# Optimization experiments

Measured on AMD Instinct MI355X. Metric: run time of the kernel, lower is better.

## Reference

```python
import jax, jax.numpy as jnp
import numpy as np

B, H0, W0, C, NH, WS, SHIFT = 32, 48, 48, 384, 12, 12, 6
N = WS * WS
TAB = 2 * WS - 1  # 23


def _window_partition(x, ws):
    b, h, w, c = x.shape
    x = x.reshape(b, h // ws, ws, w // ws, ws, c)
    return x.transpose(0, 1, 3, 2, 4, 5).reshape(-1, ws, ws, c)


def _window_reverse(win, ws, h, w):
    b = win.shape[0] // (h * w // ws // ws)
    x = win.reshape(b, h // ws, w // ws, ws, ws, -1)
    return x.transpose(0, 1, 3, 2, 4, 5).reshape(b, h, w, -1)


def _ln(y, g, b):
    m = y.mean(-1, keepdims=True)
    v = y.var(-1, keepdims=True)
    return (y - m) * jax.lax.rsqrt(v + 1e-5) * g + b


def setup_inputs() -> dict:
    key = jax.random.key(0)
    ks = jax.random.split(key, 12)
    s = 0.02
    # relative coords table, normalized to [-1, 1]
    rng = np.arange(-(WS - 1), WS, dtype=np.float32) / (WS - 1)
    table = np.stack(np.meshgrid(rng, rng, indexing='ij'), axis=-1)[None]  # (1,23,23,2)
    # relative position index
    ch, cw = np.meshgrid(np.arange(WS), np.arange(WS), indexing='ij')
    coords = np.stack([ch, cw]).reshape(2, -1)
    rel = coords[:, :, None] - coords[:, None, :] + (WS - 1)
    rpi = (rel[0] * TAB + rel[1]).astype(np.int32)  # (N,N)
    # shifted-window attention mask
    img = np.zeros((1, H0, W0, 1), dtype=np.float32)
    cnt = 0
    sl = (slice(0, -WS), slice(-WS, -SHIFT), slice(-SHIFT, None))
    for hs in sl:
        for ws_ in sl:
            img[:, hs, ws_, :] = cnt
            cnt += 1
    mw = img.reshape(1, H0 // WS, WS, W0 // WS, WS, 1).transpose(0, 1, 3, 2, 4, 5).reshape(-1, N)
    diff = mw[:, None, :] - mw[:, :, None]
    attn_mask = np.where(diff != 0, -100.0, 0.0).astype(np.float32)  # (nW,N,N)
    Ch = C * 4
    return {
        'x': jax.random.normal(ks[0], (B, H0 * W0, C), jnp.float32),
        'relative_coords_table': jnp.asarray(table),
        'relative_position_index': jnp.asarray(rpi),
        'attn_mask': jnp.asarray(attn_mask),
        'qkv_w': jax.random.normal(ks[1], (C, 3 * C), jnp.float32) * s,
        'q_bias': jnp.zeros((C,), jnp.float32),
        'v_bias': jnp.zeros((C,), jnp.float32),
        'logit_scale': jnp.log(10.0 * jnp.ones((NH, 1, 1), jnp.float32)),
        'cpb_w1': jax.random.normal(ks[2], (2, 512), jnp.float32) * s,
        'cpb_b1': jnp.zeros((512,), jnp.float32),
        'cpb_w2': jax.random.normal(ks[3], (512, NH), jnp.float32) * s,
        'proj_w': jax.random.normal(ks[4], (C, C), jnp.float32) * s,
        'proj_b': jnp.zeros((C,), jnp.float32),
        'norm1_g': jnp.ones((C,), jnp.float32),
        'norm1_b': jnp.zeros((C,), jnp.float32),
        'norm2_g': jnp.ones((C,), jnp.float32),
        'norm2_b': jnp.zeros((C,), jnp.float32),
        'fc1_w': jax.random.normal(ks[5], (C, Ch), jnp.float32) * s,
        'fc1_b': jnp.zeros((Ch,), jnp.float32),
        'fc2_w': jax.random.normal(ks[6], (Ch, C), jnp.float32) * s,
        'fc2_b': jnp.zeros((C,), jnp.float32),
        'H': H0,
        'W': W0,
    }


def reference(x, relative_coords_table, relative_position_index, attn_mask,
              qkv_w, q_bias, v_bias, logit_scale, cpb_w1, cpb_b1, cpb_w2,
              proj_w, proj_b, norm1_g, norm1_b, norm2_g, norm2_b,
              fc1_w, fc1_b, fc2_w, fc2_b, H, W):
    b, L, c = x.shape
    hd = c // NH
    shortcut = x
    x4 = x.reshape(b, H, W, c)
    shifted = jnp.roll(x4, (-SHIFT, -SHIFT), axis=(1, 2))
    xw = _window_partition(shifted, WS).reshape(-1, N, c)  # (B_, N, C)
    qkv_bias = jnp.concatenate([q_bias, jnp.zeros_like(q_bias), v_bias])
    qkv = xw @ qkv_w + qkv_bias
    qkv = qkv.reshape(-1, N, 3, NH, hd).transpose(2, 0, 3, 1, 4)  # (3,B_,h,N,d)
    q, k, v = qkv[0], qkv[1], qkv[2]
    qn = q / jnp.maximum(jnp.linalg.norm(q, axis=-1, keepdims=True), 1e-12)
    kn = k / jnp.maximum(jnp.linalg.norm(k, axis=-1, keepdims=True), 1e-12)
    attn = jnp.einsum('bhnd,bhmd->bhnm', qn, kn)
    scale = jnp.exp(jnp.minimum(logit_scale, jnp.log(100.0)))  # clamp max=log(1/0.01)
    attn = attn * scale
    tab = jax.nn.relu(relative_coords_table @ cpb_w1 + cpb_b1) @ cpb_w2  # (1,23,23,h)
    tab = tab.reshape(-1, NH)
    bias = tab[relative_position_index.reshape(-1)].reshape(N, N, NH).transpose(2, 0, 1)
    bias = 16.0 * jax.nn.sigmoid(bias)
    attn = attn + bias[None]
    nW = attn_mask.shape[0]
    attn = attn.reshape(b, nW, NH, N, N) + attn_mask[None, :, None]
    attn = jax.nn.softmax(attn.reshape(-1, NH, N, N), axis=-1)
    out = jnp.einsum('bhnm,bhmd->bhnd', attn, v).transpose(0, 2, 1, 3).reshape(-1, N, c)
    out = out @ proj_w + proj_b
    out = _window_reverse(out.reshape(-1, WS, WS, c), WS, H, W)
    x4 = jnp.roll(out, (SHIFT, SHIFT), axis=(1, 2)).reshape(b, H * W, c)
    x = shortcut + _ln(x4, norm1_g, norm1_b)
    h = jax.nn.gelu(x @ fc1_w + fc1_b, approximate=False) @ fc2_w + fc2_b
    x = x + _ln(h, norm2_g, norm2_b)
    return x
```

## Files before the change

### kernel.cpp

```cpp
#include <hip/hip_runtime.h>


typedef unsigned int uint32;
typedef unsigned short u16;
typedef __attribute__((ext_vector_type(4))) float f32x4;
typedef __attribute__((ext_vector_type(8))) __bf16 bf16x8;

static __device__ __forceinline__ u16 f2bf(float f) {
    union { float f; uint32 u; } v; v.f = f;
    uint32 r = v.u + 0x7fffu + ((v.u >> 16) & 1u);
    return (u16)(r >> 16);
}
static __device__ __forceinline__ float bf2f(u16 h) {
    union { uint32 u; float f; } v; v.u = ((uint32)h) << 16; return v.f;
}
static __device__ __forceinline__ uint32 pack2(float a, float b) {
    return (uint32)f2bf(a) | ((uint32)f2bf(b) << 16);
}
static __device__ __forceinline__ float blo(uint32 u){ union{uint32 u;float f;}v; v.u=u<<16; return v.f; }
static __device__ __forceinline__ float bhi(uint32 u){ union{uint32 u;float f;}v; v.u=u&0xffff0000u; return v.f; }

typedef __attribute__((address_space(1))) const void gas_void;
typedef __attribute__((address_space(3))) void las_void;
static __device__ __forceinline__ void glds16(const void* g, void* l) {
    __builtin_amdgcn_global_load_lds((gas_void*)g, (las_void*)l, 16, 0, 0);
}

#define SWZ(c, row) ((c) ^ ((((row) >> 1) & 3) << 3))

static __device__ __forceinline__ float fast_gelu(float x) {
    float z = x * 0.70710678118654752f;
    float az = fabsf(z);
    float t = __builtin_amdgcn_rcpf(fmaf(0.3275911f, az, 1.0f));
    float p = t * (0.254829592f + t * (-0.284496736f + t * (1.421413741f
              + t * (-1.453152027f + t * 1.061405429f))));
    float e = __expf(-z * z);
    float er = copysignf(fmaf(-p, e, 1.0f), z);
    return 0.5f * x * (1.0f + er);
}


__global__ void wt_convert(const float* __restrict__ W, u16* __restrict__ WT, int K, int N) {
    long idx = (long)blockIdx.x * 256 + threadIdx.x;
    long tot = (long)K * N;
    if (idx >= tot) return;
    int n = (int)(idx / K), k = (int)(idx - (long)n * K);
    WT[(long)n * K + SWZ(k, n)] = f2bf(W[(long)k * N + n]);
}

__global__ void build_qkv_bias(const float* __restrict__ qb, const float* __restrict__ vb,
                               float* __restrict__ outb) {
    int c = blockIdx.x * 256 + threadIdx.x;
    if (c >= 1152) return;
    outb[c] = (c < 384) ? qb[c] : ((c < 768) ? 0.f : vb[c - 768]);
}

__global__ void cpb_tab(const float* __restrict__ table, const float* __restrict__ w1,
                        const float* __restrict__ b1, const float* __restrict__ w2,
                        float* __restrict__ tab) {
    __shared__ float hid[512];
    int e = blockIdx.x;
    float tx = table[e * 2 + 0], ty = table[e * 2 + 1];
    for (int u = threadIdx.x; u < 512; u += 256)
        hid[u] = fmaxf(tx * w1[u] + ty * w1[512 + u] + b1[u], 0.f);
    __syncthreads();
    if (threadIdx.x < 12) {
        float s = 0.f;
        for (int u = 0; u < 512; ++u) s += hid[u] * w2[u * 12 + threadIdx.x];
        tab[e * 12 + threadIdx.x] = s;
    }
}

__global__ void cpb_bias(const float* __restrict__ tab, const int* __restrict__ rpi,
                         float* __restrict__ bias16) {
    int idx = blockIdx.x * 256 + threadIdx.x;
    if (idx >= 12 * 144 * 144) return;
    int h = idx / 20736, ij = idx - h * 20736;
    float t = tab[rpi[ij] * 12 + h];
    bias16[idx] = 16.f / (1.f + __expf(-t));
}

__global__ void gather_xbf(const float* __restrict__ x, u16* __restrict__ xw) {
    int idx = blockIdx.x * 256 + threadIdx.x;
    if (idx >= 73728 * 48) return;
    int row = idx / 48, c = (idx - row * 48) * 8;
    int win = row / 144, n = row - win * 144;
    int b = win >> 4, wi = win & 15;
    int r = n / 12, cc = n - r * 12;
    int sh = ((wi >> 2) * 12 + r + 6) % 48;
    int sw = ((wi & 3) * 12 + cc + 6) % 48;
    long src = ((long)(b * 2304 + sh * 48 + sw)) * 384 + c;
    float4 f0 = *(const float4*)(x + src);
    float4 f1 = *(const float4*)(x + src + 4);
    uint4 o;
    o.x = pack2(f0.x, f0.y); o.y = pack2(f0.z, f0.w);
    o.z = pack2(f1.x, f1.y); o.w = pack2(f1.z, f1.w);
    *(uint4*)(xw + (long)row * 384 + SWZ(c, row)) = o;
}


enum { EPI_QKV = 0, EPI_PLAIN = 1, EPI_GELU = 2 };

template<int EPI, bool OSWZ>
__global__ __launch_bounds__(256) void gemm_k(
    const u16* __restrict__ Ag, const u16* __restrict__ Bg,
    const float* __restrict__ bias, u16* __restrict__ outp,
    int N, int K, int ntn)
{
    __shared__ __align__(16) u16 As[2][128 * 32];
    __shared__ __align__(16) u16 Bs[2][128 * 32];
    const int tid = threadIdx.x, lane = tid & 63, wid = tid >> 6;
    const int qq = gridDim.x >> 3;
    const int wg = (blockIdx.x & 7) * qq + (blockIdx.x >> 3);
    const int mIdx = wg / ntn, nIdx = wg - mIdx * ntn;
    const int m0 = mIdx << 7, n0 = nIdx << 7;

    const int wrow = (wid >> 1) << 6, wcol = (wid & 1) << 6;
    const int fr = lane & 15, gsel = lane >> 4;

    const int s_r = (wid << 5) + (lane >> 2);
    const int s_g = (lane & 3) << 3;
    const long a_base = (long)(m0 + s_r) * K + s_g;
    const long b_base = (long)(n0 + s_r) * K + s_g;
    const long qstep = (long)16 * K;

    auto stage = [&](int buf, int kt) {
        const int k0 = kt << 5;
#pragma unroll
        for (int q = 0; q < 2; ++q) {
            glds16(Ag + a_base + qstep * q + k0, &As[buf][(wid * 32 + q * 16) * 32]);
            glds16(Bg + b_base + qstep * q + k0, &Bs[buf][(wid * 32 + q * 16) * 32]);
        }
    };

    int arow[4], acol[4], brow[4], bcol[4];
#pragma unroll
    for (int i = 0; i < 4; ++i) {
        arow[i] = wrow + i * 16 + fr; acol[i] = SWZ(gsel * 8, arow[i]);
        brow[i] = wcol + i * 16 + fr; bcol[i] = SWZ(gsel * 8, brow[i]);
    }

    f32x4 acc[4][4];
    const f32x4 zero4 = {0.f, 0.f, 0.f, 0.f};
#pragma unroll
    for (int i = 0; i < 4; ++i)
#pragma unroll
        for (int j = 0; j < 4; ++j) acc[i][j] = zero4;

    const int nk = K >> 5;
    stage(0, 0);
    int cur = 0;
    for (int kt = 0; kt < nk; ++kt) {
        __syncthreads();
        if (kt + 1 < nk) stage(cur ^ 1, kt + 1);
        bf16x8 af[4], bg[4];
#pragma unroll
        for (int i = 0; i < 4; ++i) af[i] = *(const bf16x8*)&As[cur][arow[i] * 32 + acol[i]];
#pragma unroll
        for (int j = 0; j < 4; ++j) bg[j] = *(const bf16x8*)&Bs[cur][brow[j] * 32 + bcol[j]];
#pragma unroll
        for (int i = 0; i < 4; ++i)
#pragma unroll
            for (int j = 0; j < 4; ++j)
                acc[i][j] = __builtin_amdgcn_mfma_f32_16x16x32_bf16(af[i], bg[j], acc[i][j], 0, 0, 0);
        cur ^= 1;
    }

    const int rbase = (lane >> 4) << 2;
    if constexpr (EPI == EPI_QKV) {
        long coloff[4];
        float bv[4];
#pragma unroll
        for (int j = 0; j < 4; ++j) {
            int gn0 = n0 + wcol + j * 16;
            int which = gn0 / 384;
            int c = gn0 - which * 384;
            coloff[j] = (long)(which * 12 + (c >> 5)) * 4608 + (c & 31);
            bv[j] = bias[gn0 + fr];
        }
#pragma unroll
        for (int i = 0; i < 4; ++i) {
            long rowoff[4];
#pragma unroll
            for (int r = 0; r < 4; ++r) {
                int gm = m0 + wrow + i * 16 + rbase + r;
                int win = gm / 144, n = gm - win * 144;
                rowoff[r] = (long)win * 165888 + n * 32;
            }
#pragma unroll
            for (int j = 0; j < 4; ++j)
#pragma unroll
                for (int r = 0; r < 4; ++r)
                    outp[rowoff[r] + coloff[j] + fr] = f2bf(acc[i][j][r] + bv[j]);
        }
    } else {
        float bv[4];
#pragma unroll
        for (int j = 0; j < 4; ++j) bv[j] = bias[n0 + wcol + j * 16 + fr];
#pragma unroll
        for (int i = 0; i < 4; ++i) {
#pragma unroll
            for (int r = 0; r < 4; ++r) {
                const int gm = m0 + wrow + i * 16 + rbase + r;
                u16* orow = outp + (long)gm * N;
                const int sx = OSWZ ? (((gm >> 1) & 3) << 3) : 0;
#pragma unroll
                for (int j = 0; j < 4; ++j) {
                    const int gn = n0 + wcol + j * 16 + fr;
                    float v = acc[i][j][r] + bv[j];
                    if constexpr (EPI == EPI_GELU) v = fast_gelu(v);
                    orow[gn ^ sx] = f2bf(v);
                }
            }
        }
    }
}


__global__ __launch_bounds__(192) void attn_k(
    const u16* __restrict__ qkv,
    const float* __restrict__ bias16,
    const float* __restrict__ mask,
    const float* __restrict__ lsc,
    u16* __restrict__ attn_o)
{
    __shared__ __align__(16) u16 KL[144][40];
    __shared__ __align__(16) u16 VT[32][168];
    __shared__ __align__(16) u16 PL[3][16][168];
    const int blk = blockIdx.x;
    const int win = blk / 12, head = blk - win * 12;
    const int tid = threadIdx.x, lane = tid & 63, wid = tid >> 6;
    const long base = ((long)win * 36 + head) * 4608;
    const u16* Qp = qkv + base;
    const u16* Kp = qkv + base + 12 * 4608;
    const u16* Vp = qkv + base + 24 * 4608;
    const float scale = __expf(fminf(lsc[head], 4.6051701859880914f));

    if (tid < 144) {
        const uint4* s = (const uint4*)(Kp + tid * 32);
        uint4 uu[4] = { s[0], s[1], s[2], s[3] };
        float f[32];
#pragma unroll
        for (int q = 0; q < 4; ++q) {
            f[q*8+0]=blo(uu[q].x); f[q*8+1]=bhi(uu[q].x);
            f[q*8+2]=blo(uu[q].y); f[q*8+3]=bhi(uu[q].y);
            f[q*8+4]=blo(uu[q].z); f[q*8+5]=bhi(uu[q].z);
            f[q*8+6]=blo(uu[q].w); f[q*8+7]=bhi(uu[q].w);
        }
        float ss = 0.f;
#pragma unroll
        for (int i = 0; i < 32; ++i) ss += f[i] * f[i];
        float inv = 1.f / fmaxf(sqrtf(ss), 1e-12f);
        uint32 pk[16];
#pragma unroll
        for (int i = 0; i < 16; ++i) pk[i] = pack2(f[2*i] * inv, f[2*i+1] * inv);
        uint4* d = (uint4*)&KL[tid][0];
        d[0] = make_uint4(pk[0], pk[1], pk[2], pk[3]);
        d[1] = make_uint4(pk[4], pk[5], pk[6], pk[7]);
        d[2] = make_uint4(pk[8], pk[9], pk[10], pk[11]);
        d[3] = make_uint4(pk[12], pk[13], pk[14], pk[15]);
        const uint4* sv = (const uint4*)(Vp + tid * 32);
        uint4 vv[4] = { sv[0], sv[1], sv[2], sv[3] };
        u16 vs[32];
#pragma unroll
        for (int q = 0; q < 4; ++q) {
            vs[q*8+0] = (u16)(vv[q].x & 0xffffu); vs[q*8+1] = (u16)(vv[q].x >> 16);
            vs[q*8+2] = (u16)(vv[q].y & 0xffffu); vs[q*8+3] = (u16)(vv[q].y >> 16);
            vs[q*8+4] = (u16)(vv[q].z & 0xffffu); vs[q*8+5] = (u16)(vv[q].z >> 16);
            vs[q*8+6] = (u16)(vv[q].w & 0xffffu); vs[q*8+7] = (u16)(vv[q].w >> 16);
        }
#pragma unroll
        for (int d2 = 0; d2 < 32; ++d2) VT[d2][tid] = vs[d2];
    }
    for (int idx = tid; idx < 512; idx += 192) VT[idx >> 4][144 + (idx & 15)] = 0;
    __syncthreads();

    const int fr = lane & 15, fk = (lane >> 4) << 3, rb = (lane >> 4) << 2;
    const int wim = win & 15;
    const f32x4 zero4 = {0.f, 0.f, 0.f, 0.f};

    for (int s = wid; s < 9; s += 3) {
        const uint4 qu = *(const uint4*)(Qp + (s * 16 + fr) * 32 + fk);
        float qf[8];
        qf[0]=blo(qu.x); qf[1]=bhi(qu.x); qf[2]=blo(qu.y); qf[3]=bhi(qu.y);
        qf[4]=blo(qu.z); qf[5]=bhi(qu.z); qf[6]=blo(qu.w); qf[7]=bhi(qu.w);
        float ss = 0.f;
#pragma unroll
        for (int i = 0; i < 8; ++i) ss += qf[i] * qf[i];
        ss += __shfl_xor(ss, 16);
        ss += __shfl_xor(ss, 32);
        float qinv = scale / fmaxf(sqrtf(ss), 1e-12f);
        union { uint32 u[4]; bf16x8 v; } cv;
#pragma unroll
        for (int i = 0; i < 4; ++i) cv.u[i] = pack2(qf[2*i] * qinv, qf[2*i+1] * qinv);
        bf16x8 aq = cv.v;

        f32x4 sacc[9];
#pragma unroll
        for (int jt = 0; jt < 9; ++jt) sacc[jt] = zero4;
#pragma unroll
        for (int jt = 0; jt < 9; ++jt) {
            bf16x8 bk = *(const bf16x8*)&KL[jt * 16 + fr][fk];
            sacc[jt] = __builtin_amdgcn_mfma_f32_16x16x32_bf16(aq, bk, sacc[jt], 0, 0, 0);
        }
        float mx[4] = {-1e30f, -1e30f, -1e30f, -1e30f};
#pragma unroll
        for (int jt = 0; jt < 9; ++jt) {
            int gj = jt * 16 + fr;
#pragma unroll
            for (int r = 0; r < 4; ++r) {
                int gi = s * 16 + rb + r;
                float v = sacc[jt][r] + bias16[(head * 144 + gi) * 144 + gj]
                                      + mask[(wim * 144 + gi) * 144 + gj];
                sacc[jt][r] = v;
                mx[r] = fmaxf(mx[r], v);
            }
        }
#pragma unroll
        for (int r = 0; r < 4; ++r) {
#pragma unroll
            for (int o = 1; o < 16; o <<= 1) mx[r] = fmaxf(mx[r], __shfl_xor(mx[r], o));
        }
        float sm[4] = {0.f, 0.f, 0.f, 0.f};
#pragma unroll
        for (int jt = 0; jt < 9; ++jt)
#pragma unroll
            for (int r = 0; r < 4; ++r) {
                float e = __expf(sacc[jt][r] - mx[r]);
                sacc[jt][r] = e;
                sm[r] += e;
            }
#pragma unroll
        for (int r = 0; r < 4; ++r) {
#pragma unroll
            for (int o = 1; o < 16; o <<= 1) sm[r] += __shfl_xor(sm[r], o);
            sm[r] = 1.f / sm[r];
        }
#pragma unroll
        for (int jt = 0; jt < 9; ++jt)
#pragma unroll
            for (int r = 0; r < 4; ++r)
                PL[wid][rb + r][jt * 16 + fr] = f2bf(sacc[jt][r]);
#pragma unroll
        for (int r = 0; r < 4; ++r) PL[wid][rb + r][144 + fr] = 0;

        f32x4 oa0 = zero4, oa1 = zero4;
#pragma unroll
        for (int kt = 0; kt < 5; ++kt) {
            bf16x8 ap  = *(const bf16x8*)&PL[wid][fr][kt * 32 + fk];
            bf16x8 bv0 = *(const bf16x8*)&VT[fr][kt * 32 + fk];
            bf16x8 bv1 = *(const bf16x8*)&VT[16 + fr][kt * 32 + fk];
            oa0 = __builtin_amdgcn_mfma_f32_16x16x32_bf16(ap, bv0, oa0, 0, 0, 0);
            oa1 = __builtin_amdgcn_mfma_f32_16x16x32_bf16(ap, bv1, oa1, 0, 0, 0);
        }
#pragma unroll
        for (int r = 0; r < 4; ++r) {
            long row = (long)win * 144 + s * 16 + rb + r;
            int c0 = head * 32 + fr, c1 = head * 32 + 16 + fr;
            attn_o[row * 384 + SWZ(c0, row)] = f2bf(oa0[r] * sm[r]);
            attn_o[row * 384 + SWZ(c1, row)] = f2bf(oa1[r] * sm[r]);
        }
    }
}


__global__ __launch_bounds__(256) void ln1_k(
    const u16* __restrict__ pin, const float* __restrict__ x,
    const float* __restrict__ g, const float* __restrict__ bb,
    u16* __restrict__ y1b)
{
    const int token = blockIdx.x * 4 + (threadIdx.x >> 6);
    const int lane = threadIdx.x & 63;
    int b = token / 2304, hw = token - b * 2304;
    int h = hw / 48, w = hw - h * 48;
    int sh = h + 42; if (sh >= 48) sh -= 48;
    int sw = w + 42; if (sw >= 48) sw -= 48;
    int wh = sh / 12, r = sh - wh * 12;
    int ww = sw / 12, cc = sw - ww * 12;
    long srow = (long)(b * 16 + wh * 4 + ww) * 144 + r * 12 + cc;
    const u16* src = pin + srow * 384;
    float v[6];
    {
        const ushort2* s2 = (const ushort2*)src;
#pragma unroll
        for (int i = 0; i < 3; ++i) {
            ushort2 p = s2[lane * 3 + i];
            v[i * 2] = bf2f(p.x); v[i * 2 + 1] = bf2f(p.y);
        }
    }
    float s1 = 0.f, s2 = 0.f;
#pragma unroll
    for (int i = 0; i < 6; ++i) { s1 += v[i]; s2 += v[i] * v[i]; }
#pragma unroll
    for (int o = 1; o < 64; o <<= 1) { s1 += __shfl_xor(s1, o); s2 += __shfl_xor(s2, o); }
    float mean = s1 * (1.f / 384.f);
    float var = s2 * (1.f / 384.f) - mean * mean;
    float rs = rsqrtf(var + 1e-5f);
    const float* rr = x + (long)token * 384;
    u16* oo = y1b + (long)token * 384;
#pragma unroll
    for (int i = 0; i < 6; ++i) {
        int c = lane * 6 + i;
        oo[SWZ(c, token)] = f2bf(rr[c] + (v[i] - mean) * rs * g[c] + bb[c]);
    }
}

__global__ __launch_bounds__(256) void ln2_k(
    const u16* __restrict__ t2, const u16* __restrict__ y1b,
    const float* __restrict__ g, const float* __restrict__ bb,
    float* __restrict__ outp)
{
    const int token = blockIdx.x * 4 + (threadIdx.x >> 6);
    const int lane = threadIdx.x & 63;
    const u16* src = t2 + (long)token * 384;
    float v[6];
    {
        const ushort2* s2 = (const ushort2*)src;
#pragma unroll
        for (int i = 0; i < 3; ++i) {
            ushort2 p = s2[lane * 3 + i];
            v[i * 2] = bf2f(p.x); v[i * 2 + 1] = bf2f(p.y);
        }
    }
    float s1 = 0.f, s2 = 0.f;
#pragma unroll
    for (int i = 0; i < 6; ++i) { s1 += v[i]; s2 += v[i] * v[i]; }
#pragma unroll
    for (int o = 1; o < 64; o <<= 1) { s1 += __shfl_xor(s1, o); s2 += __shfl_xor(s2, o); }
    float mean = s1 * (1.f / 384.f);
    float var = s2 * (1.f / 384.f) - mean * mean;
    float rs = rsqrtf(var + 1e-5f);
    const u16* rr = y1b + (long)token * 384;
    float* oo = outp + (long)token * 384;
#pragma unroll
    for (int i = 0; i < 6; ++i) {
        int c = lane * 6 + i;
        oo[c] = bf2f(rr[SWZ(c, token)]) + (v[i] - mean) * rs * g[c] + bb[c];
    }
}


extern "C" void kernel_launch(void* const* d_in, const int* in_sizes, int n_in,
                              void* d_out, int out_size, void* d_ws, size_t ws_size,
                              hipStream_t stream) {
    (void)in_sizes; (void)n_in; (void)out_size; (void)ws_size;
    const float* x      = (const float*)d_in[0];
    const float* table  = (const float*)d_in[1];
    const int*   rpi    = (const int*)d_in[2];
    const float* mask   = (const float*)d_in[3];
    const float* qkv_w  = (const float*)d_in[4];
    const float* q_bias = (const float*)d_in[5];
    const float* v_bias = (const float*)d_in[6];
    const float* lsc    = (const float*)d_in[7];
    const float* cpb_w1 = (const float*)d_in[8];
    const float* cpb_b1 = (const float*)d_in[9];
    const float* cpb_w2 = (const float*)d_in[10];
    const float* proj_w = (const float*)d_in[11];
    const float* proj_b = (const float*)d_in[12];
    const float* n1g    = (const float*)d_in[13];
    const float* n1b    = (const float*)d_in[14];
    const float* n2g    = (const float*)d_in[15];
    const float* n2b    = (const float*)d_in[16];
    const float* fc1_w  = (const float*)d_in[17];
    const float* fc1_b  = (const float*)d_in[18];
    const float* fc2_w  = (const float*)d_in[19];
    const float* fc2_b  = (const float*)d_in[20];
    float* outp = (float*)d_out;

    char* ws = (char*)d_ws;
    const size_t offA    = 0;
    const size_t offB    = 226492416;
    const size_t offC    = offB + 56623104;
    const size_t offBias = offC + 56623104;
    const size_t offTab  = offBias + 995328;
    const size_t offQW   = offTab + 25600;
    const size_t offPW   = offQW + 884736;
    const size_t offF1   = offPW + 294912;
    const size_t offF2   = offF1 + 1179648;
    const size_t offQB   = offF2 + 1179648;

    u16*   qkvb    = (u16*)(ws + offA);
    u16*   proj_o  = (u16*)(ws + offA);
    u16*   hbuf    = (u16*)(ws + offA);
    u16*   attn_o  = (u16*)(ws + offB);
    u16*   t2      = (u16*)(ws + offB);
    u16*   xw      = (u16*)(ws + offC);
    u16*   y1b     = (u16*)(ws + offC);
    float* bias16  = (float*)(ws + offBias);
    float* tab     = (float*)(ws + offTab);
    u16*   qkv_wT  = (u16*)(ws + offQW);
    u16*   proj_wT = (u16*)(ws + offPW);
    u16*   fc1_wT  = (u16*)(ws + offF1);
    u16*   fc2_wT  = (u16*)(ws + offF2);
    float* qkvbias = (float*)(ws + offQB);

    wt_convert<<<(384 * 1152 + 255) / 256, 256, 0, stream>>>(qkv_w, qkv_wT, 384, 1152);
    wt_convert<<<(384 * 384 + 255) / 256, 256, 0, stream>>>(proj_w, proj_wT, 384, 384);
    wt_convert<<<(384 * 1536 + 255) / 256, 256, 0, stream>>>(fc1_w, fc1_wT, 384, 1536);
    wt_convert<<<(1536 * 384 + 255) / 256, 256, 0, stream>>>(fc2_w, fc2_wT, 1536, 384);
    build_qkv_bias<<<5, 256, 0, stream>>>(q_bias, v_bias, qkvbias);
    cpb_tab<<<529, 256, 0, stream>>>(table, cpb_w1, cpb_b1, cpb_w2, tab);
    cpb_bias<<<(12 * 144 * 144 + 255) / 256, 256, 0, stream>>>(tab, rpi, bias16);
    gather_xbf<<<(73728 * 48 + 255) / 256, 256, 0, stream>>>(x, xw);

    gemm_k<EPI_QKV, false><<<576 * 9, 256, 0, stream>>>(xw, qkv_wT, qkvbias, qkvb, 1152, 384, 9);

    attn_k<<<6144, 192, 0, stream>>>(qkvb, bias16, mask, lsc, attn_o);

    gemm_k<EPI_PLAIN, false><<<576 * 3, 256, 0, stream>>>(attn_o, proj_wT, proj_b, proj_o, 384, 384, 3);

    ln1_k<<<18432, 256, 0, stream>>>(proj_o, x, n1g, n1b, y1b);

    gemm_k<EPI_GELU, true><<<576 * 12, 256, 0, stream>>>(y1b, fc1_wT, fc1_b, hbuf, 1536, 384, 12);

    gemm_k<EPI_PLAIN, false><<<576 * 3, 256, 0, stream>>>(hbuf, fc2_wT, fc2_b, t2, 384, 1536, 3);

    ln2_k<<<18432, 256, 0, stream>>>(t2, y1b, n2g, n2b, outp);
}
```

Before: 816.8 us.

## Replace GEMM with 256x256-tile 8-wave pipelined kernel and padded weights

```diff
diff --git a/kernel.cpp b/kernel.cpp
--- a/kernel.cpp
+++ b/kernel.cpp
@@ -26,7 +26,10 @@
     __builtin_amdgcn_global_load_lds((gas_void*)g, (las_void*)l, 16, 0, 0);
 }
 
-#define SWZ(c, row) ((c) ^ ((((row) >> 1) & 3) << 3))
+#define SWZ(c, row) ((c) ^ (((row) & 7) << 3))
+
+#define VMCNT(N) asm volatile("s_waitcnt vmcnt(" #N ")" ::: "memory")
+#define BARM() do { asm volatile("" ::: "memory"); __builtin_amdgcn_s_barrier(); asm volatile("" ::: "memory"); } while (0)
 
 static __device__ __forceinline__ float fast_gelu(float x) {
     float z = x * 0.70710678118654752f;
@@ -40,19 +43,21 @@
 }
 
 
-__global__ void wt_convert(const float* __restrict__ W, u16* __restrict__ WT, int K, int N) {
+__global__ void wt_convert(const float* __restrict__ W, u16* __restrict__ WT,
+                           int K, int Nreal, int Npad) {
     long idx = (long)blockIdx.x * 256 + threadIdx.x;
-    long tot = (long)K * N;
+    long tot = (long)K * Npad;
     if (idx >= tot) return;
     int n = (int)(idx / K), k = (int)(idx - (long)n * K);
-    WT[(long)n * K + SWZ(k, n)] = f2bf(W[(long)k * N + n]);
+    float v = (n < Nreal) ? W[(long)k * Nreal + n] : 0.f;
+    WT[(long)n * K + SWZ(k, n)] = f2bf(v);
 }
 
 __global__ void build_qkv_bias(const float* __restrict__ qb, const float* __restrict__ vb,
                                float* __restrict__ outb) {
     int c = blockIdx.x * 256 + threadIdx.x;
-    if (c >= 1152) return;
-    outb[c] = (c < 384) ? qb[c] : ((c < 768) ? 0.f : vb[c - 768]);
+    if (c >= 1280) return;
+    outb[c] = (c < 384) ? qb[c] : ((c < 768) ? 0.f : (c < 1152 ? vb[c - 768] : 0.f));
 }
 
 __global__ void cpb_tab(const float* __restrict__ table, const float* __restrict__ w1,
@@ -102,118 +107,156 @@
 enum { EPI_QKV = 0, EPI_PLAIN = 1, EPI_GELU = 2 };
 
 template<int EPI, bool OSWZ>
-__global__ __launch_bounds__(256) void gemm_k(
+__global__ __launch_bounds__(512, 2) void gemm8(
     const u16* __restrict__ Ag, const u16* __restrict__ Bg,
     const float* __restrict__ bias, u16* __restrict__ outp,
-    int N, int K, int ntn)
+    int Nout, int K, int ntn)
 {
-    __shared__ __align__(16) u16 As[2][128 * 32];
-    __shared__ __align__(16) u16 Bs[2][128 * 32];
+    extern __shared__ u16 lds[];
     const int tid = threadIdx.x, lane = tid & 63, wid = tid >> 6;
     const int qq = gridDim.x >> 3;
     const int wg = (blockIdx.x & 7) * qq + (blockIdx.x >> 3);
     const int mIdx = wg / ntn, nIdx = wg - mIdx * ntn;
-    const int m0 = mIdx << 7, n0 = nIdx << 7;
-
-    const int wrow = (wid >> 1) << 6, wcol = (wid & 1) << 6;
+    const int m0 = mIdx << 8, n0 = nIdx << 8;
+    const int wr = wid >> 2, wc = wid & 3;
     const int fr = lane & 15, gsel = lane >> 4;
-
-    const int s_r = (wid << 5) + (lane >> 2);
-    const int s_g = (lane & 3) << 3;
-    const long a_base = (long)(m0 + s_r) * K + s_g;
-    const long b_base = (long)(n0 + s_r) * K + s_g;
-    const long qstep = (long)16 * K;
-
-    auto stage = [&](int buf, int kt) {
-        const int k0 = kt << 5;
-#pragma unroll
-        for (int q = 0; q < 2; ++q) {
-            glds16(Ag + a_base + qstep * q + k0, &As[buf][(wid * 32 + q * 16) * 32]);
-            glds16(Bg + b_base + qstep * q + k0, &Bs[buf][(wid * 32 + q * 16) * 32]);
+    const int sx = (fr & 7) << 3;
+
+    bf16x8 a[4][2], b[2][2];
+    f32x4 acc00[4][2], acc01[4][2], acc10[4][2], acc11[4][2];
+    const f32x4 z4 = {0.f, 0.f, 0.f, 0.f};
+#pragma unroll
+    for (int i = 0; i < 4; ++i)
+#pragma unroll
+        for (int j = 0; j < 2; ++j) { acc00[i][j] = z4; acc01[i][j] = z4; acc10[i][j] = z4; acc11[i][j] = z4; }
+
+    auto STA = [&](int buf, int t, int half) {
+#pragma unroll
+        for (int u = 0; u < 2; ++u) {
+            const int g = (wid << 1) + u;
+            const int rin = half * 128 + (g << 3) + (lane >> 3);
+            glds16(Ag + (long)(m0 + rin) * K + (t << 6) + ((lane & 7) << 3),
+                   &lds[buf * 16384 + (half * 128 + (g << 3)) * 64]);
         }
     };
-
-    int arow[4], acol[4], brow[4], bcol[4];
-#pragma unroll
-    for (int i = 0; i < 4; ++i) {
-        arow[i] = wrow + i * 16 + fr; acol[i] = SWZ(gsel * 8, arow[i]);
-        brow[i] = wcol + i * 16 + fr; bcol[i] = SWZ(gsel * 8, brow[i]);
-    }
-
-    f32x4 acc[4][4];
-    const f32x4 zero4 = {0.f, 0.f, 0.f, 0.f};
-#pragma unroll
-    for (int i = 0; i < 4; ++i)
-#pragma unroll
-        for (int j = 0; j < 4; ++j) acc[i][j] = zero4;
-
-    const int nk = K >> 5;
-    stage(0, 0);
-    int cur = 0;
-    for (int kt = 0; kt < nk; ++kt) {
-        __syncthreads();
-        if (kt + 1 < nk) stage(cur ^ 1, kt + 1);
-        bf16x8 af[4], bg[4];
-#pragma unroll
-        for (int i = 0; i < 4; ++i) af[i] = *(const bf16x8*)&As[cur][arow[i] * 32 + acol[i]];
-#pragma unroll
-        for (int j = 0; j < 4; ++j) bg[j] = *(const bf16x8*)&Bs[cur][brow[j] * 32 + bcol[j]];
+    auto STB = [&](int buf, int t, int half) {
+#pragma unroll
+        for (int u = 0; u < 2; ++u) {
+            const int g = (wid << 1) + u;
+            const int rin = half * 128 + (g << 3) + (lane >> 3);
+            glds16(Bg + (long)(n0 + rin) * K + (t << 6) + ((lane & 7) << 3),
+                   &lds[32768 + buf * 16384 + (half * 128 + (g << 3)) * 64]);
+        }
+    };
+    auto RDA = [&](int buf, int mh) {
+        const int rb = mh * 128 + wr * 64 + fr;
+#pragma unroll
+        for (int i = 0; i < 4; ++i) {
+            const int r = rb + i * 16;
+#pragma unroll
+            for (int kk = 0; kk < 2; ++kk)
+                a[i][kk] = *(const bf16x8*)&lds[buf * 16384 + r * 64 + (((kk << 5) | (gsel << 3)) ^ sx)];
+        }
+    };
+    auto RDB = [&](int buf, int nh) {
+        const int rb = nh * 128 + wc * 32 + fr;
+#pragma unroll
+        for (int j = 0; j < 2; ++j) {
+            const int r = rb + j * 16;
+#pragma unroll
+            for (int kk = 0; kk < 2; ++kk)
+                b[j][kk] = *(const bf16x8*)&lds[32768 + buf * 16384 + r * 64 + (((kk << 5) | (gsel << 3)) ^ sx)];
+        }
+    };
+    auto MM = [&](f32x4 (&cc)[4][2]) {
+        __builtin_amdgcn_s_setprio(1);
 #pragma unroll
         for (int i = 0; i < 4; ++i)
 #pragma unroll
-            for (int j = 0; j < 4; ++j)
-                acc[i][j] = __builtin_amdgcn_mfma_f32_16x16x32_bf16(af[i], bg[j], acc[i][j], 0, 0, 0);
-        cur ^= 1;
-    }
-
-    const int rbase = (lane >> 4) << 2;
-    if constexpr (EPI == EPI_QKV) {
-        long coloff[4];
-        float bv[4];
-#pragma unroll
-        for (int j = 0; j < 4; ++j) {
-            int gn0 = n0 + wcol + j * 16;
-            int which = gn0 / 384;
-            int c = gn0 - which * 384;
-            coloff[j] = (long)(which * 12 + (c >> 5)) * 4608 + (c & 31);
-            bv[j] = bias[gn0 + fr];
+            for (int j = 0; j < 2; ++j)
+#pragma unroll
+                for (int kk = 0; kk < 2; ++kk)
+                    cc[i][j] = __builtin_amdgcn_mfma_f32_16x16x32_bf16(a[i][kk], b[j][kk], cc[i][j], 0, 0, 0);
+        __builtin_amdgcn_s_setprio(0);
+    };
+
+#define GITER(T, S5, W5, W6, W7)                                   \
+    STA(1, (T) + 1, 0); VMCNT(6); BARM();                          \
+    RDA(0, 0); RDB(0, 0); MM(acc00);                               \
+    STB(1, (T) + 1, 0); VMCNT(6); BARM();                          \
+    RDB(0, 1); MM(acc01);                                          \
+    STB(1, (T) + 1, 1); VMCNT(6); BARM();                          \
+    RDA(0, 1); MM(acc11);                                          \
+    STA(1, (T) + 1, 1); VMCNT(6); BARM();                          \
+    RDB(0, 0); MM(acc10);                                          \
+    if (S5) STA(0, (T) + 2, 0);                                    \
+    W5; BARM();                                                    \
+    RDA(1, 0); RDB(1, 0); MM(acc00);                               \
+    if (S5) STB(0, (T) + 2, 0);                                    \
+    W6; BARM();                                                    \
+    RDB(1, 1); MM(acc01);                                          \
+    if (S5) STB(0, (T) + 2, 1);                                    \
+    W7; BARM();                                                    \
+    RDA(1, 1); MM(acc11);                                          \
+    if (S5) STA(0, (T) + 2, 1);                                    \
+    BARM();                                                        \
+    RDB(1, 0); MM(acc10);
+
+    STA(0, 0, 0); STB(0, 0, 0); STB(0, 0, 1); STA(0, 0, 1);
+    const int niter = K >> 7;
+    for (int it = 0; it < niter - 1; ++it) {
+        const int t = it << 1;
+        GITER(t, true, VMCNT(6), VMCNT(6), VMCNT(6));
+    }
+    {
+        const int t = (niter - 1) << 1;
+        GITER(t, false, VMCNT(4), VMCNT(2), VMCNT(0));
+    }
+#undef GITER
+
+    const int rb4 = gsel << 2;
+    auto EPIL = [&](f32x4 (&cc)[4][2], int mh, int nh) {
+        int gn0[2]; bool inb[2]; float bv[2]; long coloff[2];
+#pragma unroll
+        for (int j = 0; j < 2; ++j) {
+            gn0[j] = n0 + nh * 128 + wc * 32 + j * 16;
+            inb[j] = gn0[j] < Nout;
+            bv[j] = inb[j] ? bias[gn0[j] + fr] : 0.f;
+            if (EPI == EPI_QKV && inb[j]) {
+                int which = gn0[j] / 384;
+                int c0 = gn0[j] - which * 384;
+                coloff[j] = (long)(which * 12 + (c0 >> 5)) * 4608 + (c0 & 31) + fr;
+            }
         }
 #pragma unroll
         for (int i = 0; i < 4; ++i) {
-            long rowoff[4];
 #pragma unroll
             for (int r = 0; r < 4; ++r) {
-                int gm = m0 + wrow + i * 16 + rbase + r;
-                int win = gm / 144, n = gm - win * 144;
-                rowoff[r] = (long)win * 165888 + n * 32;
-            }
-#pragma unroll
-            for (int j = 0; j < 4; ++j)
-#pragma unroll
-                for (int r = 0; r < 4; ++r)
-                    outp[rowoff[r] + coloff[j] + fr] = f2bf(acc[i][j][r] + bv[j]);
-        }
-    } else {
-        float bv[4];
-#pragma unroll
-        for (int j = 0; j < 4; ++j) bv[j] = bias[n0 + wcol + j * 16 + fr];
-#pragma unroll
-        for (int i = 0; i < 4; ++i) {
-#pragma unroll
-            for (int r = 0; r < 4; ++r) {
-                const int gm = m0 + wrow + i * 16 + rbase + r;
-                u16* orow = outp + (long)gm * N;
-                const int sx = OSWZ ? (((gm >> 1) & 3) << 3) : 0;
-#pragma unroll
-                for (int j = 0; j < 4; ++j) {
-                    const int gn = n0 + wcol + j * 16 + fr;
-                    float v = acc[i][j][r] + bv[j];
-                    if constexpr (EPI == EPI_GELU) v = fast_gelu(v);
-                    orow[gn ^ sx] = f2bf(v);
+                const int gm = m0 + mh * 128 + wr * 64 + i * 16 + rb4 + r;
+                if constexpr (EPI == EPI_QKV) {
+                    const int win = gm / 144, n = gm - win * 144;
+                    const long rowbase = (long)win * 165888 + n * 32;
+#pragma unroll
+                    for (int j = 0; j < 2; ++j)
+                        if (inb[j]) outp[rowbase + coloff[j]] = f2bf(cc[i][j][r] + bv[j]);
+                } else {
+                    u16* orow = outp + (long)gm * Nout;
+                    const int sxo = OSWZ ? ((gm & 7) << 3) : 0;
+#pragma unroll
+                    for (int j = 0; j < 2; ++j) {
+                        if (!inb[j]) continue;
+                        float v = cc[i][j][r] + bv[j];
+                        if constexpr (EPI == EPI_GELU) v = fast_gelu(v);
+                        orow[(gn0[j] + fr) ^ sxo] = f2bf(v);
+                    }
                 }
             }
         }
-    }
+    };
+    EPIL(acc00, 0, 0);
+    EPIL(acc01, 0, 1);
+    EPIL(acc10, 1, 0);
+    EPIL(acc11, 1, 1);
 }
 
 
@@ -474,10 +517,10 @@
     const size_t offBias = offC + 56623104;
     const size_t offTab  = offBias + 995328;
     const size_t offQW   = offTab + 25600;
-    const size_t offPW   = offQW + 884736;
-    const size_t offF1   = offPW + 294912;
+    const size_t offPW   = offQW + 983040;
+    const size_t offF1   = offPW + 393216;
     const size_t offF2   = offF1 + 1179648;
-    const size_t offQB   = offF2 + 1179648;
+    const size_t offQB   = offF2 + 1572864;
 
     u16*   qkvb    = (u16*)(ws + offA);
     u16*   proj_o  = (u16*)(ws + offA);
@@ -494,26 +537,33 @@
     u16*   fc2_wT  = (u16*)(ws + offF2);
     float* qkvbias = (float*)(ws + offQB);
 
-    wt_convert<<<(384 * 1152 + 255) / 256, 256, 0, stream>>>(qkv_w, qkv_wT, 384, 1152);
-    wt_convert<<<(384 * 384 + 255) / 256, 256, 0, stream>>>(proj_w, proj_wT, 384, 384);
-    wt_convert<<<(384 * 1536 + 255) / 256, 256, 0, stream>>>(fc1_w, fc1_wT, 384, 1536);
-    wt_convert<<<(1536 * 384 + 255) / 256, 256, 0, stream>>>(fc2_w, fc2_wT, 1536, 384);
+    hipFuncSetAttribute((const void*)&gemm8<EPI_QKV, false>,
+                        hipFuncAttributeMaxDynamicSharedMemorySize, 131072);
+    hipFuncSetAttribute((const void*)&gemm8<EPI_PLAIN, false>,
+                        hipFuncAttributeMaxDynamicSharedMemorySize, 131072);
+    hipFuncSetAttribute((const void*)&gemm8<EPI_GELU, true>,
+                        hipFuncAttributeMaxDynamicSharedMemorySize, 131072);
+
+    wt_convert<<<(384 * 1280 + 255) / 256, 256, 0, stream>>>(qkv_w, qkv_wT, 384, 1152, 1280);
+    wt_convert<<<(384 * 512 + 255) / 256, 256, 0, stream>>>(proj_w, proj_wT, 384, 384, 512);
+    wt_convert<<<(384 * 1536 + 255) / 256, 256, 0, stream>>>(fc1_w, fc1_wT, 384, 1536, 1536);
+    wt_convert<<<(1536 * 512 + 255) / 256, 256, 0, stream>>>(fc2_w, fc2_wT, 1536, 384, 512);
     build_qkv_bias<<<5, 256, 0, stream>>>(q_bias, v_bias, qkvbias);
     cpb_tab<<<529, 256, 0, stream>>>(table, cpb_w1, cpb_b1, cpb_w2, tab);
     cpb_bias<<<(12 * 144 * 144 + 255) / 256, 256, 0, stream>>>(tab, rpi, bias16);
     gather_xbf<<<(73728 * 48 + 255) / 256, 256, 0, stream>>>(x, xw);
 
-    gemm_k<EPI_QKV, false><<<576 * 9, 256, 0, stream>>>(xw, qkv_wT, qkvbias, qkvb, 1152, 384, 9);
+    gemm8<EPI_QKV, false><<<288 * 5, 512, 131072, stream>>>(xw, qkv_wT, qkvbias, qkvb, 1152, 384, 5);
 
     attn_k<<<6144, 192, 0, stream>>>(qkvb, bias16, mask, lsc, attn_o);
 
-    gemm_k<EPI_PLAIN, false><<<576 * 3, 256, 0, stream>>>(attn_o, proj_wT, proj_b, proj_o, 384, 384, 3);
+    gemm8<EPI_PLAIN, false><<<288 * 2, 512, 131072, stream>>>(attn_o, proj_wT, proj_b, proj_o, 384, 384, 2);
 
     ln1_k<<<18432, 256, 0, stream>>>(proj_o, x, n1g, n1b, y1b);
 
-    gemm_k<EPI_GELU, true><<<576 * 12, 256, 0, stream>>>(y1b, fc1_wT, fc1_b, hbuf, 1536, 384, 12);
-
-    gemm_k<EPI_PLAIN, false><<<576 * 3, 256, 0, stream>>>(hbuf, fc2_wT, fc2_b, t2, 384, 1536, 3);
+    gemm8<EPI_GELU, true><<<288 * 6, 512, 131072, stream>>>(y1b, fc1_wT, fc1_b, hbuf, 1536, 384, 6);
+
+    gemm8<EPI_PLAIN, false><<<288 * 2, 512, 131072, stream>>>(hbuf, fc2_wT, fc2_b, t2, 384, 1536, 2);
 
     ln2_k<<<18432, 256, 0, stream>>>(t2, y1b, n2g, n2b, outp);
 }
```

New measurement: 1.003 ms. +22.9%, slower.
